# Kernel optimization log

Measured on AMD Instinct MI355X. Metric: run time of the kernel, lower is better.

Reference implementation:

```python
import jax, jax.numpy as jnp
import numpy as np

B, S, P, N = 256, 128, 100, 500
E, H, L, F = 256, 4, 2, 1024   # embed, heads, layers, ffn
V, U, I = 50000, 10000, 10000


def setup_inputs() -> dict:
    key = jax.random.key(0)
    ks = jax.random.split(key, 32)
    u = lambda k, shp: jax.random.uniform(k, shp, jnp.float32, -0.1, 0.1)
    n = lambda k, shp, s=0.02: jax.random.normal(k, shp, jnp.float32) * s
    inp = {
        'attr': jax.random.randint(ks[0], (B, S), 0, V),
        'attr_inds': jax.random.randint(ks[1], (B, S), 0, S),
        'attr_tf': jax.random.uniform(ks[2], (B, S), jnp.float32),
        'attr_feat': jax.random.normal(ks[3], (B, 13), jnp.float32),
        'attr_lens': jax.random.randint(ks[4], (B,), S // 2, S + 1).at[0].set(S),
        'attr_lens_user': jax.random.randint(ks[5], (B,), 0, S),
        'attr_lens_item': jax.random.randint(ks[6], (B,), 0, S),
        'user_ids': jax.random.randint(ks[7], (B,), 0, U),
        'item_ids': jax.random.randint(ks[8], (B,), 0, I),
        'pos_targets': jax.random.randint(ks[9], (B, P), 0, V),
        'pos_lens': jax.random.randint(ks[10], (B,), 1, P + 1).at[0].set(P),
        'neg_targets': jax.random.randint(ks[11], (B, N), 0, V),
        'neg_lens': jax.random.randint(ks[12], (B,), 1, N + 1).at[0].set(N),
        # parameters (init_uniform(-0.1,0.1) like f_init_weight)
        'attr_emb': u(ks[13], (V, E)),
        'user_emb': u(ks[14], (U, E)),
        'item_emb': u(ks[15], (I, E)),
        'out_emb': u(ks[16], (V, 3 * E)),
        'fw_W': n(ks[17], (1, 13), 0.1),
        'fw_b': jnp.zeros((1,), jnp.float32),
        'qkv_w': n(ks[18], (L, 3 * E, E)),
        'qkv_b': jnp.zeros((L, 3 * E), jnp.float32),
        'attn_out_w': n(ks[19], (L, E, E)),
        'attn_out_b': jnp.zeros((L, E), jnp.float32),
        'ln1_s': jnp.ones((L, E), jnp.float32),
        'ln1_b': jnp.zeros((L, E), jnp.float32),
        'ff1_w': n(ks[20], (L, F, E)),
        'ff1_b': jnp.zeros((L, F), jnp.float32),
        'ff2_w': n(ks[21], (L, E, F)),
        'ff2_b': jnp.zeros((L, E), jnp.float32),
        'ln2_s': jnp.ones((L, E), jnp.float32),
        'ln2_b': jnp.zeros((L, E), jnp.float32),
    }
    return inp


def _ln(x, s, b, eps=1e-5):
    m = jnp.mean(x, axis=-1, keepdims=True)
    v = jnp.mean(jnp.square(x - m), axis=-1, keepdims=True)
    return (x - m) * jax.lax.rsqrt(v + eps) * s + b


def _encoder_layer(x, pad, p):
    # PyTorch TransformerEncoderLayer (post-norm, relu, dropout=0/eval)
    b, s, e = x.shape
    hd = e // H
    qkv = x @ p['qkv_w'].T + p['qkv_b']                      # [B,S,3E]
    q, k, v = jnp.split(qkv, 3, axis=-1)
    q = q.reshape(b, s, H, hd)
    k = k.reshape(b, s, H, hd)
    v = v.reshape(b, s, H, hd)
    scores = jnp.einsum('bqhd,bkhd->bhqk', q, k) / jnp.sqrt(jnp.float32(hd))
    scores = scores + jnp.where(pad[:, None, None, :], -1e9, 0.0)
    a = jax.nn.softmax(scores, axis=-1)
    o = jnp.einsum('bhqk,bkhd->bqhd', a, v).reshape(b, s, e)
    o = o @ p['attn_out_w'].T + p['attn_out_b']
    x = _ln(x + o, p['ln1_s'], p['ln1_b'])
    h = jax.nn.relu(x @ p['ff1_w'].T + p['ff1_b'])
    h = h @ p['ff2_w'].T + p['ff2_b']
    return _ln(x + h, p['ln2_s'], p['ln2_b'])


def reference(attr, attr_inds, attr_tf, attr_feat, attr_lens, attr_lens_user,
              attr_lens_item, user_ids, item_ids, pos_targets, pos_lens,
              neg_targets, neg_lens, attr_emb, user_emb, item_emb, out_emb,
              fw_W, fw_b, qkv_w, qkv_b, attn_out_w, attn_out_b, ln1_s, ln1_b,
              ff1_w, ff1_b, ff2_w, ff2_b, ln2_s, ln2_b):
    b, s = attr.shape
    pos = jnp.arange(s)
    pad = pos[None, :] >= attr_lens[:, None]                 # True = padding
    x = attr_emb[attr]                                       # [B,S,E]
    for l in range(qkv_w.shape[0]):
        p = {'qkv_w': qkv_w[l], 'qkv_b': qkv_b[l],
             'attn_out_w': attn_out_w[l], 'attn_out_b': attn_out_b[l],
             'ln1_s': ln1_s[l], 'ln1_b': ln1_b[l],
             'ff1_w': ff1_w[l], 'ff1_b': ff1_b[l],
             'ff2_w': ff2_w[l], 'ff2_b': ff2_b[l],
             'ln2_s': ln2_s[l], 'ln2_b': ln2_b[l]}
        x = _encoder_layer(x, pad, p)
    # per-sample scalar user weight; vectorized ragged user/item tf weighting
    w_user = jax.nn.sigmoid(attr_feat @ fw_W.T + fw_b)[:, 0]           # [B]
    side = jnp.where(pos[None, :] < attr_lens_user[:, None],
                     w_user[:, None], 1.0 - w_user[:, None])           # [B,S]
    weight = attr_tf * side * (~pad)                                   # [B,S]
    attr_x = jnp.einsum('bs,bse->be', weight, x)                       # [B,E]
    output = jnp.concatenate([user_emb[user_ids], attr_x,
                              item_emb[item_ids]], axis=-1)            # [B,3E]
    pos_logits = jnp.einsum('bpe,be->bp', out_emb[pos_targets], output)
    neg_logits = jnp.einsum('bne,be->bn', out_emb[neg_targets], output)
    pos_valid = jnp.arange(pos_targets.shape[1])[None, :] < pos_lens[:, None]
    neg_valid = jnp.arange(neg_targets.shape[1])[None, :] < neg_lens[:, None]
    logits = jnp.concatenate([pos_logits, neg_logits], axis=-1)
    mask = jnp.concatenate([pos_valid, neg_valid], axis=-1)
    new_targets = jnp.concatenate([jnp.ones_like(pos_targets),
                                   jnp.zeros_like(neg_targets)], axis=1)
    new_targets = new_targets * mask.astype(new_targets.dtype)
    return logits, mask, new_targets
```

## Files before the change

kernel.cpp:

```cpp
#include <hip/hip_runtime.h>
#include <hip/hip_bf16.h>

typedef __bf16 bf16_t;
typedef __bf16 bf16x8 __attribute__((ext_vector_type(8)));
typedef __bf16 bf16x4 __attribute__((ext_vector_type(4)));
typedef float f32x4 __attribute__((ext_vector_type(4)));

#define B_ 256
#define S_ 128
#define E_ 256
#define H_ 4
#define HD_ 64
#define F_ 1024
#define TPOS_ 100
#define TNEG_ 500
#define TT_ 600
#define ROWS_ (B_ * S_)

__global__ __launch_bounds__(256) void cvtall_kernel(
        const float* __restrict__ sq, const float* __restrict__ sa,
        const float* __restrict__ s1, const float* __restrict__ s2,
        bf16_t* __restrict__ dq, bf16_t* __restrict__ da,
        bf16_t* __restrict__ d1, bf16_t* __restrict__ d2) {
    int i = blockIdx.x * 256 + threadIdx.x;
    if (i < 393216) { dq[i] = (bf16_t)sq[i]; }
    else if (i < 524288) { int j = i - 393216; da[j] = (bf16_t)sa[j]; }
    else if (i < 1048576) { int j = i - 524288; d1[j] = (bf16_t)s1[j]; }
    else { int j = i - 1048576; d2[j] = (bf16_t)s2[j]; }
}

__global__ __launch_bounds__(256) void embed_kernel(const int* __restrict__ attr,
        const float* __restrict__ emb, bf16_t* __restrict__ xb) {
    int row = blockIdx.x * 4 + (threadIdx.x >> 6);
    int lane = threadIdx.x & 63;
    int idx = attr[row];
    float4 v = reinterpret_cast<const float4*>(emb + (size_t)idx * E_)[lane];
    bf16x4 o; o[0] = (bf16_t)v.x; o[1] = (bf16_t)v.y; o[2] = (bf16_t)v.z; o[3] = (bf16_t)v.w;
    *reinterpret_cast<bf16x4*>(xb + (size_t)row * E_ + lane * 4) = o;
}

template<bool RELU>
__global__ __launch_bounds__(256) void gemm_kernel(
        const bf16_t* __restrict__ A, const bf16_t* __restrict__ W,
        const float* __restrict__ bias, bf16_t* __restrict__ outB, int M, int N, int K) {
    __shared__ bf16_t lA[2][128 * 32];
    __shared__ bf16_t lB[2][128 * 32];
    int tid = threadIdx.x;
    int wave = tid >> 6, lane = tid & 63;
    int wr = wave >> 1, wc = wave & 1;
    int mBase = blockIdx.y * 128;
    int nBase = blockIdx.x * 128;
    int r16 = lane & 15, kg = lane >> 4;

    int srow = wave * 16 + (lane >> 2);
    int scol = (lane & 3) * 8;
    const bf16_t* gA = A + (size_t)(mBase + srow) * K + scol;
    const bf16_t* gB = W + (size_t)(nBase + srow) * K + scol;
    int ldst = wave * 512;

    f32x4 acc[4][4] = {};

    #define STAGE(buf, k0) { \
        _Pragma("unroll") \
        for (int iss = 0; iss < 2; iss++) { \
            __builtin_amdgcn_global_load_lds( \
                (const __attribute__((address_space(1))) void*)(gA + (size_t)iss * 64 * K + (k0)), \
                (__attribute__((address_space(3))) void*)(&lA[buf][iss * 2048 + ldst]), 16, 0, 0); \
            __builtin_amdgcn_global_load_lds( \
                (const __attribute__((address_space(1))) void*)(gB + (size_t)iss * 64 * K + (k0)), \
                (__attribute__((address_space(3))) void*)(&lB[buf][iss * 2048 + ldst]), 16, 0, 0); \
        } }

    STAGE(0, 0);
    int cur = 0;
    for (int k0 = 0; k0 < K; k0 += 32) {
        __syncthreads();
        if (k0 + 32 < K) STAGE(cur ^ 1, k0 + 32);
        bf16x8 a[4], b[4];
        #pragma unroll
        for (int i = 0; i < 4; i++) {
            a[i] = *reinterpret_cast<const bf16x8*>(&lA[cur][(wr * 64 + i * 16 + r16) * 32 + kg * 8]);
            b[i] = *reinterpret_cast<const bf16x8*>(&lB[cur][(wc * 64 + i * 16 + r16) * 32 + kg * 8]);
        }
        #pragma unroll
        for (int mi = 0; mi < 4; mi++)
            #pragma unroll
            for (int ni = 0; ni < 4; ni++)
                acc[mi][ni] = __builtin_amdgcn_mfma_f32_16x16x32_bf16(a[mi], b[ni], acc[mi][ni], 0, 0, 0);
        cur ^= 1;
    }
    #undef STAGE

    #pragma unroll
    for (int mi = 0; mi < 4; mi++) {
        #pragma unroll
        for (int ni = 0; ni < 4; ni++) {
            int col = nBase + wc * 64 + ni * 16 + r16;
            float bv = bias[col];
            #pragma unroll
            for (int j = 0; j < 4; j++) {
                int row = mBase + wr * 64 + mi * 16 + kg * 4 + j;
                float v = acc[mi][ni][j] + bv;
                if (RELU) v = v > 0.f ? v : 0.f;
                outB[(size_t)row * N + col] = (bf16_t)v;
            }
        }
    }
}

__global__ __launch_bounds__(256) void gemm_ln_kernel(
        const bf16_t* __restrict__ A, const bf16_t* __restrict__ W,
        const float* __restrict__ bias, const float* __restrict__ sc,
        const float* __restrict__ bi, bf16_t* __restrict__ xb, int M, int K) {
    __shared__ bf16_t lA[2][64 * 32];
    __shared__ bf16_t lB[2][256 * 32];
    __shared__ float psum[64][2][2];
    int tid = threadIdx.x;
    int wave = tid >> 6, lane = tid & 63;
    int wm = wave >> 1, wn = wave & 1;
    int mBase = blockIdx.x * 64;
    int r16 = lane & 15, kg = lane >> 4;

    const bf16_t* gA = A + (size_t)(mBase + wave * 16 + (lane >> 2)) * K + (lane & 3) * 8;
    const bf16_t* gB = W + (size_t)((lane >> 2)) * K + (lane & 3) * 8;

    f32x4 acc[2][8] = {};

    #define STAGE2(buf, k0) { \
        __builtin_amdgcn_global_load_lds( \
            (const __attribute__((address_space(1))) void*)(gA + (k0)), \
            (__attribute__((address_space(3))) void*)(&lA[buf][wave * 512]), 16, 0, 0); \
        _Pragma("unroll") \
        for (int iss = 0; iss < 4; iss++) { \
            int q = wave * 4 + iss; \
            __builtin_amdgcn_global_load_lds( \
                (const __attribute__((address_space(1))) void*)(gB + (size_t)q * 16 * K + (k0)), \
                (__attribute__((address_space(3))) void*)(&lB[buf][q * 512]), 16, 0, 0); \
        } }

    STAGE2(0, 0);
    int cur = 0;
    for (int k0 = 0; k0 < K; k0 += 32) {
        __syncthreads();
        if (k0 + 32 < K) STAGE2(cur ^ 1, k0 + 32);
        bf16x8 a[2], b[8];
        #pragma unroll
        for (int mi = 0; mi < 2; mi++)
            a[mi] = *reinterpret_cast<const bf16x8*>(&lA[cur][(wm * 32 + mi * 16 + r16) * 32 + kg * 8]);
        #pragma unroll
        for (int ni = 0; ni < 8; ni++)
            b[ni] = *reinterpret_cast<const bf16x8*>(&lB[cur][(wn * 128 + ni * 16 + r16) * 32 + kg * 8]);
        #pragma unroll
        for (int mi = 0; mi < 2; mi++)
            #pragma unroll
            for (int ni = 0; ni < 8; ni++)
                acc[mi][ni] = __builtin_amdgcn_mfma_f32_16x16x32_bf16(a[mi], b[ni], acc[mi][ni], 0, 0, 0);
        cur ^= 1;
    }
    #undef STAGE2

    float bv[8];
    #pragma unroll
    for (int ni = 0; ni < 8; ni++) bv[ni] = bias[wn * 128 + ni * 16 + r16];
    #pragma unroll
    for (int mi = 0; mi < 2; mi++) {
        #pragma unroll
        for (int j = 0; j < 4; j++) {
            int rl = wm * 32 + mi * 16 + kg * 4 + j;
            const bf16_t* rrow = xb + (size_t)(mBase + rl) * 256;
            float s = 0.f, q = 0.f;
            #pragma unroll
            for (int ni = 0; ni < 8; ni++) {
                int col = wn * 128 + ni * 16 + r16;
                float v = acc[mi][ni][j] + bv[ni] + (float)rrow[col];
                acc[mi][ni][j] = v;
                s += v; q += v * v;
            }
            #pragma unroll
            for (int m = 1; m < 16; m <<= 1) { s += __shfl_xor(s, m); q += __shfl_xor(q, m); }
            if (r16 == 0) { psum[rl][wn][0] = s; psum[rl][wn][1] = q; }
        }
    }
    __syncthreads();
    #pragma unroll
    for (int mi = 0; mi < 2; mi++) {
        #pragma unroll
        for (int j = 0; j < 4; j++) {
            int rl = wm * 32 + mi * 16 + kg * 4 + j;
            float s = psum[rl][0][0] + psum[rl][1][0];
            float qq = psum[rl][0][1] + psum[rl][1][1];
            float mean = s * (1.0f / 256.0f);
            float var = qq * (1.0f / 256.0f) - mean * mean;
            float inv = rsqrtf(var + 1e-5f);
            bf16_t* orow = xb + (size_t)(mBase + rl) * 256;
            #pragma unroll
            for (int ni = 0; ni < 8; ni++) {
                int col = wn * 128 + ni * 16 + r16;
                float o = (acc[mi][ni][j] - mean) * inv * sc[col] + bi[col];
                orow[col] = (bf16_t)o;
            }
        }
    }
}

__global__ __launch_bounds__(256) void attn_kernel(const bf16_t* __restrict__ qkv,
        const int* __restrict__ lens, bf16_t* __restrict__ out) {
    __shared__ bf16_t p[S_][S_ + 8];
    __shared__ bf16_t vl[HD_][S_ + 8];
    int bh = blockIdx.x; int b = bh >> 2, h = bh & 3;
    int wave = threadIdx.x >> 6, lane = threadIdx.x & 63;
    int r16 = lane & 15, kg = lane >> 4;
    int q0 = wave * 32;
    int len = lens[b];
    const bf16_t* qbase = qkv + (size_t)b * S_ * 768;

    {
        int sl = (wave & 1) * 64 + lane;
        const bf16_t* vsrc = qbase + (size_t)sl * 768 + 512 + h * HD_;
        #pragma unroll
        for (int pass = 0; pass < 4; pass++) {
            int d0 = (pass * 2 + (wave >> 1)) * 8;
            bf16x8 v = *reinterpret_cast<const bf16x8*>(vsrc + d0);
            #pragma unroll
            for (int j = 0; j < 8; j++) vl[d0 + j][sl] = v[j];
        }
    }

    f32x4 acc[2][8] = {};
    #pragma unroll
    for (int ks = 0; ks < 2; ks++) {
        int kOff = h * HD_ + ks * 32 + kg * 8;
        bf16x8 a[2], bb[8];
        #pragma unroll
        for (int mi = 0; mi < 2; mi++)
            a[mi] = *reinterpret_cast<const bf16x8*>(qbase + (size_t)(q0 + mi * 16 + r16) * 768 + kOff);
        #pragma unroll
        for (int ni = 0; ni < 8; ni++)
            bb[ni] = *reinterpret_cast<const bf16x8*>(qbase + (size_t)(ni * 16 + r16) * 768 + 256 + kOff);
        #pragma unroll
        for (int mi = 0; mi < 2; mi++)
            #pragma unroll
            for (int ni = 0; ni < 8; ni++)
                acc[mi][ni] = __builtin_amdgcn_mfma_f32_16x16x32_bf16(a[mi], bb[ni], acc[mi][ni], 0, 0, 0);
    }
    #pragma unroll
    for (int mi = 0; mi < 2; mi++) {
        #pragma unroll
        for (int j = 0; j < 4; j++) {
            float vals[8]; float mx = -1e30f;
            #pragma unroll
            for (int ni = 0; ni < 8; ni++) {
                int kp = ni * 16 + r16;
                float v = acc[mi][ni][j] * 0.125f;
                vals[ni] = (kp < len) ? v : -1e30f;
                mx = fmaxf(mx, vals[ni]);
            }
            #pragma unroll
            for (int m = 1; m < 16; m <<= 1) mx = fmaxf(mx, __shfl_xor(mx, m));
            float sum = 0.f;
            #pragma unroll
            for (int ni = 0; ni < 8; ni++) {
                vals[ni] = (vals[ni] > -1e29f) ? __expf(vals[ni] - mx) : 0.f;
                sum += vals[ni];
            }
            #pragma unroll
            for (int m = 1; m < 16; m <<= 1) sum += __shfl_xor(sum, m);
            float inv = 1.0f / sum;
            int row = q0 + mi * 16 + kg * 4 + j;
            #pragma unroll
            for (int ni = 0; ni < 8; ni++)
                p[row][ni * 16 + r16] = (bf16_t)(vals[ni] * inv);
        }
    }
    __syncthreads();
    f32x4 acc2[2][4] = {};
    #pragma unroll
    for (int ks = 0; ks < 4; ks++) {
        int k = ks * 32 + kg * 8;
        bf16x8 a[2], bb[4];
        #pragma unroll
        for (int mi = 0; mi < 2; mi++)
            a[mi] = *reinterpret_cast<const bf16x8*>(&p[q0 + mi * 16 + r16][k]);
        #pragma unroll
        for (int ni = 0; ni < 4; ni++)
            bb[ni] = *reinterpret_cast<const bf16x8*>(&vl[ni * 16 + r16][k]);
        #pragma unroll
        for (int mi = 0; mi < 2; mi++)
            #pragma unroll
            for (int ni = 0; ni < 4; ni++)
                acc2[mi][ni] = __builtin_amdgcn_mfma_f32_16x16x32_bf16(a[mi], bb[ni], acc2[mi][ni], 0, 0, 0);
    }
    #pragma unroll
    for (int mi = 0; mi < 2; mi++)
        #pragma unroll
        for (int ni = 0; ni < 4; ni++)
            #pragma unroll
            for (int j = 0; j < 4; j++) {
                int q = q0 + mi * 16 + kg * 4 + j;
                int d = ni * 16 + r16;
                out[((size_t)b * S_ + q) * E_ + h * HD_ + d] = (bf16_t)acc2[mi][ni][j];
            }
}

__global__ void wuser_kernel(const float* __restrict__ feat, const float* __restrict__ W,
                             const float* __restrict__ bb, float* __restrict__ wu) {
    int b = threadIdx.x;
    if (b < B_) {
        float z = bb[0];
        #pragma unroll
        for (int i = 0; i < 13; i++) z += feat[b * 13 + i] * W[i];
        wu[b] = 1.f / (1.f + __expf(-z));
    }
}

__global__ __launch_bounds__(256) void pool_kernel(
        const bf16_t* __restrict__ xb, const float* __restrict__ attr_tf,
        const int* __restrict__ lens, const int* __restrict__ lens_user,
        const float* __restrict__ wu, const int* __restrict__ uid, const int* __restrict__ iid,
        const float* __restrict__ user_emb, const float* __restrict__ item_emb,
        float* __restrict__ outvec) {
    int b = blockIdx.x, t = threadIdx.x;
    __shared__ float wrow[S_];
    if (t < S_) {
        float w = (t < lens[b]) ? attr_tf[b * S_ + t] : 0.f;
        float side = (t < lens_user[b]) ? wu[b] : (1.f - wu[b]);
        wrow[t] = w * side;
    }
    __syncthreads();
    float acc = 0.f;
    const bf16_t* xr = xb + (size_t)b * S_ * E_ + t;
    #pragma unroll 4
    for (int s = 0; s < S_; s++) acc += wrow[s] * (float)xr[(size_t)s * E_];
    outvec[b * 768 + 256 + t] = acc;
    outvec[b * 768 + t] = user_emb[(size_t)uid[b] * E_ + t];
    outvec[b * 768 + 512 + t] = item_emb[(size_t)iid[b] * E_ + t];
}

__global__ __launch_bounds__(256) void logits_kernel(
        const float* __restrict__ outvec, const float* __restrict__ out_emb,
        const int* __restrict__ pos_t, const int* __restrict__ pos_l,
        const int* __restrict__ neg_t, const int* __restrict__ neg_l,
        float* __restrict__ dout) {
    int g = blockIdx.x * 4 + (threadIdx.x >> 6);
    int lane = threadIdx.x & 63;
    int b = g / TT_, t = g - b * TT_;
    int tgt, valid, ispos;
    if (t < TPOS_) { tgt = pos_t[b * TPOS_ + t]; valid = (t < pos_l[b]); ispos = 1; }
    else { int tn = t - TPOS_; tgt = neg_t[b * TNEG_ + tn]; valid = (tn < neg_l[b]); ispos = 0; }
    const float4* e4 = reinterpret_cast<const float4*>(out_emb + (size_t)tgt * 768);
    const float4* o4 = reinterpret_cast<const float4*>(outvec + (size_t)b * 768);
    float acc = 0.f;
    #pragma unroll
    for (int c = 0; c < 3; c++) {
        float4 a = e4[c * 64 + lane];
        float4 o = o4[c * 64 + lane];
        acc += a.x * o.x + a.y * o.y + a.z * o.z + a.w * o.w;
    }
    #pragma unroll
    for (int m = 1; m < 64; m <<= 1) acc += __shfl_xor(acc, m);
    if (lane == 0) {
        size_t i = (size_t)b * TT_ + t;
        dout[i] = acc;
        dout[(size_t)B_ * TT_ + i] = valid ? 1.0f : 0.0f;
        dout[2 * (size_t)B_ * TT_ + i] = (valid && ispos) ? 1.0f : 0.0f;
    }
}

extern "C" void kernel_launch(void* const* d_in, const int* in_sizes, int n_in,
                              void* d_out, int out_size, void* d_ws, size_t ws_size,
                              hipStream_t stream) {
    const int*   attr        = (const int*)d_in[0];
    const float* attr_tf     = (const float*)d_in[2];
    const float* attr_feat   = (const float*)d_in[3];
    const int*   attr_lens   = (const int*)d_in[4];
    const int*   attr_lens_u = (const int*)d_in[5];
    const int*   user_ids    = (const int*)d_in[7];
    const int*   item_ids    = (const int*)d_in[8];
    const int*   pos_targets = (const int*)d_in[9];
    const int*   pos_lens    = (const int*)d_in[10];
    const int*   neg_targets = (const int*)d_in[11];
    const int*   neg_lens    = (const int*)d_in[12];
    const float* attr_emb    = (const float*)d_in[13];
    const float* user_emb    = (const float*)d_in[14];
    const float* item_emb    = (const float*)d_in[15];
    const float* out_emb     = (const float*)d_in[16];
    const float* fw_W        = (const float*)d_in[17];
    const float* fw_b        = (const float*)d_in[18];
    const float* qkv_w       = (const float*)d_in[19];
    const float* qkv_b       = (const float*)d_in[20];
    const float* attn_out_w  = (const float*)d_in[21];
    const float* attn_out_b  = (const float*)d_in[22];
    const float* ln1_s       = (const float*)d_in[23];
    const float* ln1_b       = (const float*)d_in[24];
    const float* ff1_w       = (const float*)d_in[25];
    const float* ff1_b       = (const float*)d_in[26];
    const float* ff2_w       = (const float*)d_in[27];
    const float* ff2_b       = (const float*)d_in[28];
    const float* ln2_s       = (const float*)d_in[29];
    const float* ln2_b       = (const float*)d_in[30];

    size_t szRes = (size_t)ROWS_ * E_ * 2;
    size_t wB = (size_t)1572864 * 2;
    size_t fixedB = 2 * szRes + wB + (size_t)B_ * 768 * 4 + 4096 + 16384;
    int CH = 32;
    for (int ch = 1; ch <= 32; ch <<= 1) {
        if (fixedB + (size_t)(ROWS_ / ch) * 1024 * 2 <= ws_size) { CH = ch; break; }
    }
    int rowsC = ROWS_ / CH, sampC = B_ / CH;

    char* ws = (char*)d_ws;
    size_t off = 0;
    auto alloc = [&](size_t bytes) { void* pp = ws + off; off += (bytes + 255) & ~255ULL; return pp; };
    bf16_t* xb  = (bf16_t*)alloc(szRes);
    bf16_t* ob  = (bf16_t*)alloc(szRes);
    bf16_t* wq  = (bf16_t*)alloc((size_t)393216 * 2);
    bf16_t* wa  = (bf16_t*)alloc((size_t)131072 * 2);
    bf16_t* w1  = (bf16_t*)alloc((size_t)524288 * 2);
    bf16_t* w2  = (bf16_t*)alloc((size_t)524288 * 2);
    float* outvec = (float*)alloc((size_t)B_ * 768 * 4);
    float* wu     = (float*)alloc(1024);
    bf16_t* chunk = (bf16_t*)alloc((size_t)rowsC * 1024 * 2);

    cvtall_kernel<<<6144, 256, 0, stream>>>(qkv_w, attn_out_w, ff1_w, ff2_w, wq, wa, w1, w2);
    embed_kernel<<<ROWS_ / 4, 256, 0, stream>>>(attr, attr_emb, xb);

    for (int l = 0; l < 2; l++) {
        for (int c = 0; c < CH; c++) {
            size_t r0 = (size_t)c * rowsC;
            gemm_kernel<false><<<dim3(6, rowsC / 128), 256, 0, stream>>>(
                xb + r0 * E_, wq + (size_t)l * 768 * 256, qkv_b + l * 768, chunk, rowsC, 768, 256);
            attn_kernel<<<sampC * H_, 256, 0, stream>>>(chunk, attr_lens + c * sampC, ob + r0 * E_);
        }
        gemm_ln_kernel<<<ROWS_ / 64, 256, 0, stream>>>(
            ob, wa + (size_t)l * 256 * 256, attn_out_b + l * 256,
            ln1_s + l * 256, ln1_b + l * 256, xb, ROWS_, 256);
        for (int c = 0; c < CH; c++) {
            size_t r0 = (size_t)c * rowsC;
            gemm_kernel<true><<<dim3(8, rowsC / 128), 256, 0, stream>>>(
                xb + r0 * E_, w1 + (size_t)l * 1024 * 256, ff1_b + l * 1024, chunk, rowsC, 1024, 256);
            gemm_ln_kernel<<<rowsC / 64, 256, 0, stream>>>(
                chunk, w2 + (size_t)l * 256 * 1024, ff2_b + l * 256,
                ln2_s + l * 256, ln2_b + l * 256, xb + r0 * E_, rowsC, 1024);
        }
    }

    wuser_kernel<<<1, 256, 0, stream>>>(attr_feat, fw_W, fw_b, wu);
    pool_kernel<<<B_, 256, 0, stream>>>(xb, attr_tf, attr_lens, attr_lens_u, wu,
                                        user_ids, item_ids, user_emb, item_emb, outvec);
    logits_kernel<<<B_ * TT_ / 4, 256, 0, stream>>>(outvec, out_emb, pos_targets, pos_lens,
                                                    neg_targets, neg_lens, (float*)d_out);
}
```

Baseline: 389.4 us.

## Switch GEMMs to 32x32x16 MFMA and read output embeddings as bf16

Both GEMM kernels now use 32x32x16 bf16 MFMA tiles instead of 16x16x32, which changes the accumulator layout and the epilogue row mapping. This cuts the number of MFMA issues and LDS fragment loads per K step. Separately, a new kernel converts the whole 50000x768 out_emb table to bf16 on every call, and the logits kernel reads that copy. This halves the gather bytes in the logits kernel, but it adds a full-table read and write per call (about 150MB read and 77MB written), which may cost more than the gather traffic it saves (B*600 rows).

```diff
diff --git a/kernel.cpp b/kernel.cpp
--- a/kernel.cpp
+++ b/kernel.cpp
@@ -5,6 +5,7 @@
 typedef __bf16 bf16x8 __attribute__((ext_vector_type(8)));
 typedef __bf16 bf16x4 __attribute__((ext_vector_type(4)));
 typedef float f32x4 __attribute__((ext_vector_type(4)));
+typedef float f32x16 __attribute__((ext_vector_type(16)));
 
 #define B_ 256
 #define S_ 128
@@ -16,6 +17,7 @@
 #define TNEG_ 500
 #define TT_ 600
 #define ROWS_ (B_ * S_)
+#define VO_ (50000 * 768)
 
 __global__ __launch_bounds__(256) void cvtall_kernel(
         const float* __restrict__ sq, const float* __restrict__ sa,
@@ -27,6 +29,17 @@
     else if (i < 524288) { int j = i - 393216; da[j] = (bf16_t)sa[j]; }
     else if (i < 1048576) { int j = i - 524288; d1[j] = (bf16_t)s1[j]; }
     else { int j = i - 1048576; d2[j] = (bf16_t)s2[j]; }
+}
+
+__global__ __launch_bounds__(256) void cvt_oemb_kernel(const float* __restrict__ in,
+        bf16_t* __restrict__ out) {
+    size_t base = ((size_t)blockIdx.x * 256 + threadIdx.x) * 8;
+    float4 v0 = reinterpret_cast<const float4*>(in + base)[0];
+    float4 v1 = reinterpret_cast<const float4*>(in + base)[1];
+    bf16x8 o;
+    o[0] = (bf16_t)v0.x; o[1] = (bf16_t)v0.y; o[2] = (bf16_t)v0.z; o[3] = (bf16_t)v0.w;
+    o[4] = (bf16_t)v1.x; o[5] = (bf16_t)v1.y; o[6] = (bf16_t)v1.z; o[7] = (bf16_t)v1.w;
+    *reinterpret_cast<bf16x8*>(out + base) = o;
 }
 
 __global__ __launch_bounds__(256) void embed_kernel(const int* __restrict__ attr,
@@ -50,7 +63,7 @@
     int wr = wave >> 1, wc = wave & 1;
     int mBase = blockIdx.y * 128;
     int nBase = blockIdx.x * 128;
-    int r16 = lane & 15, kg = lane >> 4;
+    int r32 = lane & 31, kh = lane >> 5;
 
     int srow = wave * 16 + (lane >> 2);
     int scol = (lane & 3) * 8;
@@ -58,7 +71,7 @@
     const bf16_t* gB = W + (size_t)(nBase + srow) * K + scol;
     int ldst = wave * 512;
 
-    f32x4 acc[4][4] = {};
+    f32x16 acc[2][2] = {};
 
     #define STAGE(buf, k0) { \
         _Pragma("unroll") \
@@ -76,31 +89,38 @@
     for (int k0 = 0; k0 < K; k0 += 32) {
         __syncthreads();
         if (k0 + 32 < K) STAGE(cur ^ 1, k0 + 32);
-        bf16x8 a[4], b[4];
-        #pragma unroll
-        for (int i = 0; i < 4; i++) {
-            a[i] = *reinterpret_cast<const bf16x8*>(&lA[cur][(wr * 64 + i * 16 + r16) * 32 + kg * 8]);
-            b[i] = *reinterpret_cast<const bf16x8*>(&lB[cur][(wc * 64 + i * 16 + r16) * 32 + kg * 8]);
-        }
-        #pragma unroll
-        for (int mi = 0; mi < 4; mi++)
-            #pragma unroll
-            for (int ni = 0; ni < 4; ni++)
-                acc[mi][ni] = __builtin_amdgcn_mfma_f32_16x16x32_bf16(a[mi], b[ni], acc[mi][ni], 0, 0, 0);
+        bf16x8 a[2][2], b[2][2];
+        #pragma unroll
+        for (int i = 0; i < 2; i++)
+            #pragma unroll
+            for (int kk = 0; kk < 2; kk++) {
+                a[i][kk] = *reinterpret_cast<const bf16x8*>(
+                    &lA[cur][(wr * 64 + i * 32 + r32) * 32 + kk * 16 + kh * 8]);
+                b[i][kk] = *reinterpret_cast<const bf16x8*>(
+                    &lB[cur][(wc * 64 + i * 32 + r32) * 32 + kk * 16 + kh * 8]);
+            }
+        #pragma unroll
+        for (int mi = 0; mi < 2; mi++)
+            #pragma unroll
+            for (int ni = 0; ni < 2; ni++)
+                #pragma unroll
+                for (int kk = 0; kk < 2; kk++)
+                    acc[mi][ni] = __builtin_amdgcn_mfma_f32_32x32x16_bf16(
+                        a[mi][kk], b[ni][kk], acc[mi][ni], 0, 0, 0);
         cur ^= 1;
     }
     #undef STAGE
 
     #pragma unroll
-    for (int mi = 0; mi < 4; mi++) {
-        #pragma unroll
-        for (int ni = 0; ni < 4; ni++) {
-            int col = nBase + wc * 64 + ni * 16 + r16;
+    for (int mi = 0; mi < 2; mi++) {
+        #pragma unroll
+        for (int ni = 0; ni < 2; ni++) {
+            int col = nBase + wc * 64 + ni * 32 + r32;
             float bv = bias[col];
             #pragma unroll
-            for (int j = 0; j < 4; j++) {
-                int row = mBase + wr * 64 + mi * 16 + kg * 4 + j;
-                float v = acc[mi][ni][j] + bv;
+            for (int r = 0; r < 16; r++) {
+                int row = mBase + wr * 64 + mi * 32 + (r & 3) + 8 * (r >> 2) + 4 * kh;
+                float v = acc[mi][ni][r] + bv;
                 if (RELU) v = v > 0.f ? v : 0.f;
                 outB[(size_t)row * N + col] = (bf16_t)v;
             }
@@ -119,12 +139,12 @@
     int wave = tid >> 6, lane = tid & 63;
     int wm = wave >> 1, wn = wave & 1;
     int mBase = blockIdx.x * 64;
-    int r16 = lane & 15, kg = lane >> 4;
+    int r32 = lane & 31, kh = lane >> 5;
 
     const bf16_t* gA = A + (size_t)(mBase + wave * 16 + (lane >> 2)) * K + (lane & 3) * 8;
     const bf16_t* gB = W + (size_t)((lane >> 2)) * K + (lane & 3) * 8;
 
-    f32x4 acc[2][8] = {};
+    f32x16 acc[4] = {};
 
     #define STAGE2(buf, k0) { \
         __builtin_amdgcn_global_load_lds( \
@@ -143,62 +163,60 @@
     for (int k0 = 0; k0 < K; k0 += 32) {
         __syncthreads();
         if (k0 + 32 < K) STAGE2(cur ^ 1, k0 + 32);
-        bf16x8 a[2], b[8];
-        #pragma unroll
-        for (int mi = 0; mi < 2; mi++)
-            a[mi] = *reinterpret_cast<const bf16x8*>(&lA[cur][(wm * 32 + mi * 16 + r16) * 32 + kg * 8]);
-        #pragma unroll
-        for (int ni = 0; ni < 8; ni++)
-            b[ni] = *reinterpret_cast<const bf16x8*>(&lB[cur][(wn * 128 + ni * 16 + r16) * 32 + kg * 8]);
-        #pragma unroll
-        for (int mi = 0; mi < 2; mi++)
-            #pragma unroll
-            for (int ni = 0; ni < 8; ni++)
-                acc[mi][ni] = __builtin_amdgcn_mfma_f32_16x16x32_bf16(a[mi], b[ni], acc[mi][ni], 0, 0, 0);
+        bf16x8 a[2], b[4][2];
+        #pragma unroll
+        for (int kk = 0; kk < 2; kk++)
+            a[kk] = *reinterpret_cast<const bf16x8*>(
+                &lA[cur][(wm * 32 + r32) * 32 + kk * 16 + kh * 8]);
+        #pragma unroll
+        for (int ni = 0; ni < 4; ni++)
+            #pragma unroll
+            for (int kk = 0; kk < 2; kk++)
+                b[ni][kk] = *reinterpret_cast<const bf16x8*>(
+                    &lB[cur][(wn * 128 + ni * 32 + r32) * 32 + kk * 16 + kh * 8]);
+        #pragma unroll
+        for (int ni = 0; ni < 4; ni++)
+            #pragma unroll
+            for (int kk = 0; kk < 2; kk++)
+                acc[ni] = __builtin_amdgcn_mfma_f32_32x32x16_bf16(a[kk], b[ni][kk], acc[ni], 0, 0, 0);
         cur ^= 1;
     }
     #undef STAGE2
 
-    float bv[8];
-    #pragma unroll
-    for (int ni = 0; ni < 8; ni++) bv[ni] = bias[wn * 128 + ni * 16 + r16];
-    #pragma unroll
-    for (int mi = 0; mi < 2; mi++) {
-        #pragma unroll
-        for (int j = 0; j < 4; j++) {
-            int rl = wm * 32 + mi * 16 + kg * 4 + j;
-            const bf16_t* rrow = xb + (size_t)(mBase + rl) * 256;
-            float s = 0.f, q = 0.f;
-            #pragma unroll
-            for (int ni = 0; ni < 8; ni++) {
-                int col = wn * 128 + ni * 16 + r16;
-                float v = acc[mi][ni][j] + bv[ni] + (float)rrow[col];
-                acc[mi][ni][j] = v;
-                s += v; q += v * v;
-            }
-            #pragma unroll
-            for (int m = 1; m < 16; m <<= 1) { s += __shfl_xor(s, m); q += __shfl_xor(q, m); }
-            if (r16 == 0) { psum[rl][wn][0] = s; psum[rl][wn][1] = q; }
-        }
+    float bv[4];
+    #pragma unroll
+    for (int ni = 0; ni < 4; ni++) bv[ni] = bias[wn * 128 + ni * 32 + r32];
+    #pragma unroll
+    for (int r = 0; r < 16; r++) {
+        int rl = wm * 32 + (r & 3) + 8 * (r >> 2) + 4 * kh;
+        const bf16_t* rrow = xb + (size_t)(mBase + rl) * 256;
+        float s = 0.f, q = 0.f;
+        #pragma unroll
+        for (int ni = 0; ni < 4; ni++) {
+            int col = wn * 128 + ni * 32 + r32;
+            float v = acc[ni][r] + bv[ni] + (float)rrow[col];
+            acc[ni][r] = v;
+            s += v; q += v * v;
+        }
+        #pragma unroll
+        for (int m = 1; m < 32; m <<= 1) { s += __shfl_xor(s, m); q += __shfl_xor(q, m); }
+        if (r32 == 0) { psum[rl][wn][0] = s; psum[rl][wn][1] = q; }
     }
     __syncthreads();
     #pragma unroll
-    for (int mi = 0; mi < 2; mi++) {
-        #pragma unroll
-        for (int j = 0; j < 4; j++) {
-            int rl = wm * 32 + mi * 16 + kg * 4 + j;
-            float s = psum[rl][0][0] + psum[rl][1][0];
-            float qq = psum[rl][0][1] + psum[rl][1][1];
-            float mean = s * (1.0f / 256.0f);
-            float var = qq * (1.0f / 256.0f) - mean * mean;
-            float inv = rsqrtf(var + 1e-5f);
-            bf16_t* orow = xb + (size_t)(mBase + rl) * 256;
-            #pragma unroll
-            for (int ni = 0; ni < 8; ni++) {
-                int col = wn * 128 + ni * 16 + r16;
-                float o = (acc[mi][ni][j] - mean) * inv * sc[col] + bi[col];
-                orow[col] = (bf16_t)o;
-            }
+    for (int r = 0; r < 16; r++) {
+        int rl = wm * 32 + (r & 3) + 8 * (r >> 2) + 4 * kh;
+        float s = psum[rl][0][0] + psum[rl][1][0];
+        float qq = psum[rl][0][1] + psum[rl][1][1];
+        float mean = s * (1.0f / 256.0f);
+        float var = qq * (1.0f / 256.0f) - mean * mean;
+        float inv = rsqrtf(var + 1e-5f);
+        bf16_t* orow = xb + (size_t)(mBase + rl) * 256;
+        #pragma unroll
+        for (int ni = 0; ni < 4; ni++) {
+            int col = wn * 128 + ni * 32 + r32;
+            float o = (acc[ni][r] - mean) * inv * sc[col] + bi[col];
+            orow[col] = (bf16_t)o;
         }
     }
 }
@@ -337,7 +355,7 @@
 }
 
 __global__ __launch_bounds__(256) void logits_kernel(
-        const float* __restrict__ outvec, const float* __restrict__ out_emb,
+        const float* __restrict__ outvec, const bf16_t* __restrict__ oeb,
         const int* __restrict__ pos_t, const int* __restrict__ pos_l,
         const int* __restrict__ neg_t, const int* __restrict__ neg_l,
         float* __restrict__ dout) {
@@ -347,14 +365,14 @@
     int tgt, valid, ispos;
     if (t < TPOS_) { tgt = pos_t[b * TPOS_ + t]; valid = (t < pos_l[b]); ispos = 1; }
     else { int tn = t - TPOS_; tgt = neg_t[b * TNEG_ + tn]; valid = (tn < neg_l[b]); ispos = 0; }
-    const float4* e4 = reinterpret_cast<const float4*>(out_emb + (size_t)tgt * 768);
+    const bf16_t* erow = oeb + (size_t)tgt * 768;
     const float4* o4 = reinterpret_cast<const float4*>(outvec + (size_t)b * 768);
     float acc = 0.f;
     #pragma unroll
     for (int c = 0; c < 3; c++) {
-        float4 a = e4[c * 64 + lane];
+        bf16x4 a = *reinterpret_cast<const bf16x4*>(erow + c * 256 + lane * 4);
         float4 o = o4[c * 64 + lane];
-        acc += a.x * o.x + a.y * o.y + a.z * o.z + a.w * o.w;
+        acc += (float)a[0] * o.x + (float)a[1] * o.y + (float)a[2] * o.z + (float)a[3] * o.w;
     }
     #pragma unroll
     for (int m = 1; m < 64; m <<= 1) acc += __shfl_xor(acc, m);
@@ -401,7 +419,8 @@
 
     size_t szRes = (size_t)ROWS_ * E_ * 2;
     size_t wB = (size_t)1572864 * 2;
-    size_t fixedB = 2 * szRes + wB + (size_t)B_ * 768 * 4 + 4096 + 16384;
+    size_t oebB = (size_t)VO_ * 2;
+    size_t fixedB = 2 * szRes + wB + oebB + (size_t)B_ * 768 * 4 + 4096 + 16384;
     int CH = 32;
     for (int ch = 1; ch <= 32; ch <<= 1) {
         if (fixedB + (size_t)(ROWS_ / ch) * 1024 * 2 <= ws_size) { CH = ch; break; }
@@ -417,11 +436,13 @@
     bf16_t* wa  = (bf16_t*)alloc((size_t)131072 * 2);
     bf16_t* w1  = (bf16_t*)alloc((size_t)524288 * 2);
     bf16_t* w2  = (bf16_t*)alloc((size_t)524288 * 2);
+    bf16_t* oeb = (bf16_t*)alloc(oebB);
     float* outvec = (float*)alloc((size_t)B_ * 768 * 4);
     float* wu     = (float*)alloc(1024);
     bf16_t* chunk = (bf16_t*)alloc((size_t)rowsC * 1024 * 2);
 
     cvtall_kernel<<<6144, 256, 0, stream>>>(qkv_w, attn_out_w, ff1_w, ff2_w, wq, wa, w1, w2);
+    cvt_oemb_kernel<<<VO_ / (256 * 8), 256, 0, stream>>>(out_emb, oeb);
     embed_kernel<<<ROWS_ / 4, 256, 0, stream>>>(attr, attr_emb, xb);
 
     for (int l = 0; l < 2; l++) {
@@ -447,6 +468,6 @@
     wuser_kernel<<<1, 256, 0, stream>>>(attr_feat, fw_W, fw_b, wu);
     pool_kernel<<<B_, 256, 0, stream>>>(xb, attr_tf, attr_lens, attr_lens_u, wu,
                                         user_ids, item_ids, user_emb, item_emb, outvec);
-    logits_kernel<<<B_ * TT_ / 4, 256, 0, stream>>>(outvec, out_emb, pos_targets, pos_lens,
+    logits_kernel<<<B_ * TT_ / 4, 256, 0, stream>>>(outvec, oeb, pos_targets, pos_lens,
                                                     neg_targets, neg_lens, (float*)d_out);
 }
```

New measurement: 450.8 us. +15.8%, slower.
